# Optimization experiments

Hardware: AMD Instinct MI355X
Metric: run time of the kernel (lower is better)

## Reference

```python
import jax, jax.numpy as jnp
import numpy as np

B, S, H, SSZ, IN = 1024, 100, 128, 100, 2


def _gru(x, h, Wih, Whh, bih, bhh):
    # PyTorch GRU cell: gates ordered (reset, update, new)
    gx = x @ Wih.T + bih
    gh = h @ Whh.T + bhh
    xr, xz, xn = jnp.split(gx, 3, axis=-1)
    hr, hz, hn = jnp.split(gh, 3, axis=-1)
    r = jax.nn.sigmoid(xr + hr)
    z = jax.nn.sigmoid(xz + hz)
    n = jnp.tanh(xn + r * hn)
    return (1.0 - z) * n + z * h


def _attn(inst_h, rnn_out, W, v):
    # inst_h: [B,S,H], rnn_out: [B,H] -> softmax attention weights [B,S]
    h = jnp.concatenate([inst_h, jnp.broadcast_to(rnn_out[:, None, :], inst_h.shape)], axis=-1)
    s = jax.nn.relu(jnp.einsum('bsk,kh->bsh', h, W)) @ v
    return jax.nn.softmax(s, axis=1)


def setup_inputs() -> dict:
    key = jax.random.key(0)
    k = jax.random.split(key, 32)
    p = lambda i, shape, sc=0.05: sc * jax.random.normal(k[i], shape, jnp.float32)
    instance = jax.random.uniform(k[0], (B, S, IN), jnp.float32)
    # solutions must be per-row permutations of node indices
    solution_1 = jnp.argsort(jax.random.uniform(k[1], (B, S)), axis=1).astype(jnp.int32)
    solution_2 = jnp.argsort(jax.random.uniform(k[2], (B, S)), axis=1).astype(jnp.int32)
    eps = jax.random.normal(k[3], (B, SSZ), jnp.float32)
    return dict(
        instance=instance, solution_1=solution_1, solution_2=solution_2, eps=eps,
        emb_i_W=p(4, (H, IN)), emb_i_b=jnp.zeros(H, jnp.float32),
        emb_r_W=p(5, (H, IN)), emb_r_b=jnp.zeros(H, jnp.float32),
        attn_W=p(6, (2 * H, H)), attn_v=p(7, (H,)),
        gru_Wih=p(8, (3 * H, H)), gru_Whh=p(9, (3 * H, H)),
        gru_bih=jnp.zeros(3 * H, jnp.float32), gru_bhh=jnp.zeros(3 * H, jnp.float32),
        grud_Wih=p(10, (3 * H, 2 * H)), grud_Whh=p(11, (3 * H, H)),
        grud_bih=jnp.zeros(3 * H, jnp.float32), grud_bhh=jnp.zeros(3 * H, jnp.float32),
        enc_fc1_W=p(12, (SSZ, H)), enc_fc1_b=jnp.zeros(SSZ, jnp.float32),
        enc_fc2_W=p(13, (SSZ, H)), enc_fc2_b=jnp.zeros(SSZ, jnp.float32),
        ptr_W=p(14, (2 * H, H)), ptr_v=p(15, (H,)),
        pfc1_W=p(16, (2 * H, 2 * H + SSZ)), pfc1_b=jnp.zeros(2 * H, jnp.float32),
        pfc2_W=p(17, (H, 2 * H)), pfc2_b=jnp.zeros(H, jnp.float32),
    )


def reference(instance, solution_1, solution_2, eps,
              emb_i_W, emb_i_b, emb_r_W, emb_r_b, attn_W, attn_v,
              gru_Wih, gru_Whh, gru_bih, gru_bhh,
              grud_Wih, grud_Whh, grud_bih, grud_bhh,
              enc_fc1_W, enc_fc1_b, enc_fc2_W, enc_fc2_b,
              ptr_W, ptr_v, pfc1_W, pfc1_b, pfc2_W, pfc2_b):
    b_idx = jnp.arange(B)
    inst_h = instance @ emb_i_W.T + emb_i_b  # [B,S,H]
    emb_r = lambda x: x @ emb_r_W.T + emb_r_b
    take = lambda ptr: instance[b_idx, ptr]  # gather node coords [B,IN]

    # ---------------- Encoder ----------------
    def enc_step(carry, ptr):
        h1, h2, ref_h = carry
        h1 = _gru(ref_h, h1, gru_Wih, gru_Whh, gru_bih, gru_bhh)
        a = _attn(inst_h, h1, attn_W, attn_v)
        context = jnp.einsum('bs,bsh->bh', a, inst_h)
        ref_h = emb_r(take(ptr))
        rnn_in = jnp.concatenate([ref_h, context], axis=-1)  # [B,2H]
        h2 = _gru(rnn_in, h2, grud_Wih, grud_Whh, grud_bih, grud_bhh)
        return (h1, h2, ref_h), None

    z0 = jnp.zeros((B, H), instance.dtype)
    ref_h0 = emb_r(take(solution_1[:, 0]))
    (_, h2, _), _ = jax.lax.scan(enc_step, (z0, z0, ref_h0), solution_1[:, 1:].T)
    mu = h2 @ enc_fc1_W.T + enc_fc1_b
    log_var = h2 @ enc_fc2_W.T + enc_fc2_b
    Z = mu + eps * jnp.exp(0.5 * log_var)

    # ---------------- Decoder (teacher forcing) ----------------
    mask0 = jnp.ones((B, S), instance.dtype).at[b_idx, solution_2[:, 0]].set(0.0)

    def dec_step(carry, ptr):
        h1, ref_in, mask = carry
        ref_h = emb_r(ref_in)
        h1 = _gru(ref_h, h1, gru_Wih, gru_Whh, gru_bih, gru_bhh)
        a = _attn(inst_h, h1, attn_W, attn_v)
        context = jnp.einsum('bs,bsh->bh', a, inst_h)
        fc_in = jnp.concatenate([context, Z, ref_h], axis=-1)  # [B, 2H+SSZ]
        fc_out = (fc_in @ pfc1_W.T + pfc1_b) @ pfc2_W.T + pfc2_b  # no activation, as in torch
        hcat = jnp.concatenate([inst_h, jnp.broadcast_to(fc_out[:, None, :], inst_h.shape)], axis=-1)
        logits = jnp.tanh(jnp.einsum('bsk,kh->bsh', hcat, ptr_W)) @ ptr_v  # [B,S]
        probs = jax.nn.softmax(logits + jnp.log(mask), axis=1)
        logp = jnp.log(probs[b_idx, ptr])
        pred = jnp.argmax(probs, axis=1)
        mask = mask.at[b_idx, ptr].set(0.0)  # tsp.update_mask: mark chosen node visited
        return (h1, take(ptr), mask), (pred, logp)

    init = (z0, take(solution_2[:, 0]), mask0)
    _, (preds, logps) = jax.lax.scan(dec_step, init, solution_2[:, 1:].T)
    tour_idx = jnp.concatenate([solution_2[:, :1], preds.T.astype(solution_2.dtype)], axis=1)
    tour_logp = logps.T  # [B, S-1]
    return (mu, log_var, Z, tour_idx, tour_logp)
```

## Files before the change

### kernel.cpp

```cpp
#include <hip/hip_runtime.h>
#include <math.h>

static constexpr int NB  = 1024;
static constexpr int NS  = 100;
static constexpr int NH  = 128;
static constexpr int GPB = 2;
static constexpr int NTHR = 256;
static constexpr int NBLK = NB / GPB;

static constexpr int OUT_MU = 0;
static constexpr int OUT_LV = NB * NS;
static constexpr int OUT_Z  = 2 * NB * NS;
static constexpr int OUT_TI = 3 * NB * NS;
static constexpr int OUT_LP = 4 * NB * NS;

#define NEGF (-3.4e38f)

template<int C4>
__device__ __forceinline__ void dot2x3f(const float* __restrict__ wr0,
        const float* __restrict__ wr1, const float* __restrict__ wr2,
        const float* __restrict__ x0, const float* __restrict__ x1,
        float& r00, float& r01, float& r10, float& r11, float& r20, float& r21)
{
    const float4* W0 = reinterpret_cast<const float4*>(wr0);
    const float4* W1 = reinterpret_cast<const float4*>(wr1);
    const float4* W2 = reinterpret_cast<const float4*>(wr2);
    const float4* X0 = reinterpret_cast<const float4*>(x0);
    const float4* X1 = reinterpret_cast<const float4*>(x1);
    float a00 = 0.f, a01 = 0.f, a10 = 0.f, a11 = 0.f, a20 = 0.f, a21 = 0.f;
    #pragma unroll 8
    for (int c = 0; c < C4; ++c) {
        float4 u0 = W0[c], u1 = W1[c], u2 = W2[c];
        float4 v0 = X0[c], v1 = X1[c];
        a00 = fmaf(u0.x, v0.x, a00); a00 = fmaf(u0.y, v0.y, a00); a00 = fmaf(u0.z, v0.z, a00); a00 = fmaf(u0.w, v0.w, a00);
        a01 = fmaf(u0.x, v1.x, a01); a01 = fmaf(u0.y, v1.y, a01); a01 = fmaf(u0.z, v1.z, a01); a01 = fmaf(u0.w, v1.w, a01);
        a10 = fmaf(u1.x, v0.x, a10); a10 = fmaf(u1.y, v0.y, a10); a10 = fmaf(u1.z, v0.z, a10); a10 = fmaf(u1.w, v0.w, a10);
        a11 = fmaf(u1.x, v1.x, a11); a11 = fmaf(u1.y, v1.y, a11); a11 = fmaf(u1.z, v1.z, a11); a11 = fmaf(u1.w, v1.w, a11);
        a20 = fmaf(u2.x, v0.x, a20); a20 = fmaf(u2.y, v0.y, a20); a20 = fmaf(u2.z, v0.z, a20); a20 = fmaf(u2.w, v0.w, a20);
        a21 = fmaf(u2.x, v1.x, a21); a21 = fmaf(u2.y, v1.y, a21); a21 = fmaf(u2.z, v1.z, a21); a21 = fmaf(u2.w, v1.w, a21);
    }
    r00 = a00; r01 = a01; r10 = a10; r11 = a11; r20 = a20; r21 = a21;
}

template<int C4>
__device__ __forceinline__ void dot2f(const float* __restrict__ w,
        const float* __restrict__ x0, const float* __restrict__ x1, float& r0, float& r1)
{
    const float4* W = reinterpret_cast<const float4*>(w);
    const float4* X0 = reinterpret_cast<const float4*>(x0);
    const float4* X1 = reinterpret_cast<const float4*>(x1);
    float a0 = 0.f, a1 = 0.f;
    #pragma unroll 8
    for (int c = 0; c < C4; ++c) {
        float4 u = W[c];
        float4 v0 = X0[c], v1 = X1[c];
        a0 = fmaf(u.x, v0.x, a0); a0 = fmaf(u.y, v0.y, a0); a0 = fmaf(u.z, v0.z, a0); a0 = fmaf(u.w, v0.w, a0);
        a1 = fmaf(u.x, v1.x, a1); a1 = fmaf(u.y, v1.y, a1); a1 = fmaf(u.z, v1.z, a1); a1 = fmaf(u.w, v1.w, a1);
    }
    r0 = a0; r1 = a1;
}

template<int C4>
__device__ __forceinline__ void dot1f(const float* __restrict__ w,
        const float* __restrict__ x0, float& r0)
{
    const float4* W = reinterpret_cast<const float4*>(w);
    const float4* X0 = reinterpret_cast<const float4*>(x0);
    float a0 = 0.f;
    #pragma unroll 8
    for (int c = 0; c < C4; ++c) {
        float4 u = W[c];
        float4 v0 = X0[c];
        a0 = fmaf(u.x, v0.x, a0); a0 = fmaf(u.y, v0.y, a0); a0 = fmaf(u.z, v0.z, a0); a0 = fmaf(u.w, v0.w, a0);
    }
    r0 = a0;
}

template<int C4>
__device__ __forceinline__ double dotwd(const float* __restrict__ w, const float* __restrict__ x)
{
    const float4* W = reinterpret_cast<const float4*>(w);
    double a = 0.0;
    #pragma unroll 8
    for (int c = 0; c < C4; ++c) {
        float4 u = W[c];
        const float* p = x + 4 * c;
        a = fma((double)u.x, (double)p[0], a);
        a = fma((double)u.y, (double)p[1], a);
        a = fma((double)u.z, (double)p[2], a);
        a = fma((double)u.w, (double)p[3], a);
    }
    return a;
}

__device__ __forceinline__ void gruc(const float* __restrict__ bih, const float* __restrict__ bhh,
        const float* __restrict__ pa, const float* __restrict__ pb, float* __restrict__ h, int j)
{
    double r = 1.0 / (1.0 + exp(-(((double)pa[j]        + (double)bih[j])        + ((double)pb[j]        + (double)bhh[j]))));
    double z = 1.0 / (1.0 + exp(-(((double)pa[NH + j]   + (double)bih[NH + j])   + ((double)pb[NH + j]   + (double)bhh[NH + j]))));
    double n = tanh(((double)pa[2*NH + j] + (double)bih[2*NH + j]) + r * ((double)pb[2*NH + j] + (double)bhh[2*NH + j]));
    h[j] = (float)((1.0 - z) * n + z * (double)h[j]);
}

__global__ __launch_bounds__(NTHR) void vae_v14(
    const float* __restrict__ instance, const int* __restrict__ sol1,
    const int* __restrict__ sol2, const float* __restrict__ eps,
    const float* __restrict__ emb_i_W, const float* __restrict__ emb_i_b,
    const float* __restrict__ emb_r_W, const float* __restrict__ emb_r_b,
    const float* __restrict__ attn_W, const float* __restrict__ attn_v,
    const float* __restrict__ gru_Wih, const float* __restrict__ gru_Whh,
    const float* __restrict__ gru_bih, const float* __restrict__ gru_bhh,
    const float* __restrict__ grud_Wih, const float* __restrict__ grud_Whh,
    const float* __restrict__ grud_bih, const float* __restrict__ grud_bhh,
    const float* __restrict__ efc1_W, const float* __restrict__ efc1_b,
    const float* __restrict__ efc2_W, const float* __restrict__ efc2_b,
    const float* __restrict__ ptr_W, const float* __restrict__ ptr_v,
    const float* __restrict__ pfc1_W, const float* __restrict__ pfc1_b,
    const float* __restrict__ pfc2_W, const float* __restrict__ pfc2_b,
    float* __restrict__ out)
{
    __shared__ float  s_x[GPB][360];
    __shared__ float  s_h1[GPB][NH], s_h2[GPB][NH], s_fco[GPB][NH];
    __shared__ float  s_fch[GPB][256];
    __shared__ float  s_pa[GPB][3 * NH], s_pb[GPB][3 * NH];
    __shared__ double s_qh[GPB][NH];
    __shared__ double s_qpA[GPB][NH], s_qpB[GPB][NH];
    __shared__ double2 dAa[NH], dAp[NH];
    __shared__ double dAba[NH], dAbp[NH];
    __shared__ float  s_lg[GPB][NS], s_a[GPB][NS];
    __shared__ float  s_c0[GPB][NS], s_c1[GPB][NS], s_msk[GPB][NS];
    __shared__ float  t_wi0[NH], t_wi1[NH], t_bi[NH];
    __shared__ float  t_wr0[NH], t_wr1[NH], t_br[NH];
    __shared__ float  t_va[NH], t_vp[NH];
    __shared__ float  t_gbih[3*NH], t_gbhh[3*NH], t_dbih[3*NH], t_dbhh[3*NH];
    __shared__ float  t_p1b[256], t_p2b[NH];
    __shared__ int    s_sol1[GPB][NS], s_sol2[GPB][NS];
    __shared__ float  s_red[GPB][2];
    __shared__ double s_redd[GPB][2];
    __shared__ int    s_ri[GPB][2];
    __shared__ float  s_rc0[GPB], s_rc1[GPB];

    const int tid = threadIdx.x;
    const int bbase = blockIdx.x * GPB;
    const int j = tid & (NH - 1);
    const int half = tid >> 7;
    const int g = half;
    const int lane = tid & 63;
    const int wid = (tid >> 6) & 1;

    if (tid < NH) {
        t_wi0[tid] = emb_i_W[2*tid]; t_wi1[tid] = emb_i_W[2*tid+1]; t_bi[tid] = emb_i_b[tid];
        t_wr0[tid] = emb_r_W[2*tid]; t_wr1[tid] = emb_r_W[2*tid+1]; t_br[tid] = emb_r_b[tid];
        t_va[tid] = attn_v[tid]; t_vp[tid] = ptr_v[tid];
        t_p2b[tid] = pfc2_b[tid];
    }
    t_p1b[tid] = pfc1_b[tid];
    for (int i = tid; i < 3 * NH; i += NTHR) {
        t_gbih[i] = gru_bih[i]; t_gbhh[i] = gru_bhh[i];
        t_dbih[i] = grud_bih[i]; t_dbhh[i] = grud_bhh[i];
    }
    for (int i = tid; i < GPB * NS; i += NTHR) {
        int gg = i / NS, s = i - gg * NS;
        s_c0[gg][s] = instance[(size_t)((bbase + gg) * NS + s) * 2 + 0];
        s_c1[gg][s] = instance[(size_t)((bbase + gg) * NS + s) * 2 + 1];
        s_sol1[gg][s] = sol1[(bbase + gg) * NS + s];
        s_sol2[gg][s] = sol2[(bbase + gg) * NS + s];
    }
    s_h1[g][j] = 0.f;
    s_h2[g][j] = 0.f;
    __syncthreads();
    {
        const float* Wm = (half == 0) ? attn_W : ptr_W;
        double a0 = 0.0, a1 = 0.0, ab = 0.0;
        for (int k = 0; k < NH; ++k) {
            double wv = (double)Wm[(size_t)k * NH + j];
            a0 = fma((double)t_wi0[k], wv, a0);
            a1 = fma((double)t_wi1[k], wv, a1);
            ab = fma((double)t_bi[k],  wv, ab);
        }
        if (half == 0) { dAa[j].x = a0; dAa[j].y = a1; dAba[j] = ab; }
        else           { dAp[j].x = a0; dAp[j].y = a1; dAbp[j] = ab; }
    }
    {
        int sp = s_sol1[g][0];
        s_x[g][j] = fmaf(s_c0[g][sp], t_wr0[j], fmaf(s_c1[g][sp], t_wr1[j], t_br[j]));
    }
    __syncthreads();

    for (int t = 1; t < NS; ++t) {
        if (half == 0) {
            float a00,a01,a10,a11,a20,a21;
            dot2x3f<32>(gru_Wih + (size_t)j * NH, gru_Wih + (size_t)(NH + j) * NH,
                        gru_Wih + (size_t)(2*NH + j) * NH, s_x[0], s_x[1],
                        a00,a01,a10,a11,a20,a21);
            s_pa[0][j] = a00;        s_pa[1][j] = a01;
            s_pa[0][NH + j] = a10;   s_pa[1][NH + j] = a11;
            s_pa[0][2*NH + j] = a20; s_pa[1][2*NH + j] = a21;
        } else {
            float a00,a01,a10,a11,a20,a21;
            dot2x3f<32>(gru_Whh + (size_t)j * NH, gru_Whh + (size_t)(NH + j) * NH,
                        gru_Whh + (size_t)(2*NH + j) * NH, s_h1[0], s_h1[1],
                        a00,a01,a10,a11,a20,a21);
            s_pb[0][j] = a00;        s_pb[1][j] = a01;
            s_pb[0][NH + j] = a10;   s_pb[1][NH + j] = a11;
            s_pb[0][2*NH + j] = a20; s_pb[1][2*NH + j] = a21;
        }
        __syncthreads();
        gruc(t_gbih, t_gbhh, s_pa[g], s_pb[g], s_h1[g], j);
        __syncthreads();
        {
            const float* col = attn_W + (size_t)NH * NH + j;
            const int k0 = half * 64;
            double a00=0.0,a01=0.0,a02=0.0,a03=0.0;
            double a10=0.0,a11=0.0,a12=0.0,a13=0.0;
            #pragma unroll 8
            for (int k = 0; k < 64; k += 4) {
                float w0 = col[(size_t)(k0+k+0) * NH];
                float w1 = col[(size_t)(k0+k+1) * NH];
                float w2 = col[(size_t)(k0+k+2) * NH];
                float w3 = col[(size_t)(k0+k+3) * NH];
                float4 h0 = *reinterpret_cast<const float4*>(&s_h1[0][k0+k]);
                float4 h1v = *reinterpret_cast<const float4*>(&s_h1[1][k0+k]);
                a00 = fma((double)w0, (double)h0.x, a00);
                a01 = fma((double)w1, (double)h0.y, a01);
                a02 = fma((double)w2, (double)h0.z, a02);
                a03 = fma((double)w3, (double)h0.w, a03);
                a10 = fma((double)w0, (double)h1v.x, a10);
                a11 = fma((double)w1, (double)h1v.y, a11);
                a12 = fma((double)w2, (double)h1v.z, a12);
                a13 = fma((double)w3, (double)h1v.w, a13);
            }
            if (half == 0) { s_qpA[0][j] = (a00+a01)+(a02+a03); s_qpA[1][j] = (a10+a11)+(a12+a13); }
            else           { s_qpB[0][j] = (a00+a01)+(a02+a03); s_qpB[1][j] = (a10+a11)+(a12+a13); }
        }
        __syncthreads();
        s_qh[g][j] = dAba[j] + (s_qpA[g][j] + s_qpB[g][j]);
        __syncthreads();
        if (j < NS) {
            double c00 = (double)s_c0[g][j], c10 = (double)s_c1[g][j];
            double acc0 = 0.0, acc1 = 0.0, acc2 = 0.0, acc3 = 0.0;
            #pragma unroll 4
            for (int h = 0; h < NH; h += 4) {
                double2 A0 = dAa[h+0], A1 = dAa[h+1], A2 = dAa[h+2], A3 = dAa[h+3];
                double p0 = fma(c00, A0.x, fma(c10, A0.y, s_qh[g][h+0]));
                double p1 = fma(c00, A1.x, fma(c10, A1.y, s_qh[g][h+1]));
                double p2 = fma(c00, A2.x, fma(c10, A2.y, s_qh[g][h+2]));
                double p3 = fma(c00, A3.x, fma(c10, A3.y, s_qh[g][h+3]));
                acc0 = fma(fmax(p0, 0.0), (double)t_va[h+0], acc0);
                acc1 = fma(fmax(p1, 0.0), (double)t_va[h+1], acc1);
                acc2 = fma(fmax(p2, 0.0), (double)t_va[h+2], acc2);
                acc3 = fma(fmax(p3, 0.0), (double)t_va[h+3], acc3);
            }
            s_lg[g][j] = (float)(((acc0 + acc1) + (acc2 + acc3)));
        }
        __syncthreads();
        {
            float a = s_lg[g][lane];
            float b = (lane + 64 < NS) ? s_lg[g][lane + 64] : NEGF;
            float m = fmaxf(a, b);
            m = fmaxf(m, __shfl_xor(m, 32)); m = fmaxf(m, __shfl_xor(m, 16));
            m = fmaxf(m, __shfl_xor(m, 8));  m = fmaxf(m, __shfl_xor(m, 4));
            m = fmaxf(m, __shfl_xor(m, 2));  m = fmaxf(m, __shfl_xor(m, 1));
            float fv = 0.f;
            if (j < NS) { fv = (float)exp((double)s_lg[g][j] - (double)m); s_a[g][j] = fv; }
            double ps = (double)fv;
            ps += __shfl_xor(ps, 32); ps += __shfl_xor(ps, 16);
            ps += __shfl_xor(ps, 8);  ps += __shfl_xor(ps, 4);
            ps += __shfl_xor(ps, 2);  ps += __shfl_xor(ps, 1);
            if (lane == 0) s_redd[g][wid] = ps;
        }
        __syncthreads();
        if (j < NS) {
            double se = s_redd[g][0] + s_redd[g][1];
            s_a[g][j] = (float)((double)s_a[g][j] / se);
        }
        __syncthreads();
        {
            float w0 = t_wi0[j], w1 = t_wi1[j], bb = t_bi[j];
            double a0 = 0.0, a1 = 0.0, a2 = 0.0, a3 = 0.0;
            #pragma unroll 5
            for (int s = 0; s < NS; s += 4) {
                float ih0 = fmaf(s_c0[g][s+0], w0, fmaf(s_c1[g][s+0], w1, bb));
                float ih1 = fmaf(s_c0[g][s+1], w0, fmaf(s_c1[g][s+1], w1, bb));
                float ih2 = fmaf(s_c0[g][s+2], w0, fmaf(s_c1[g][s+2], w1, bb));
                float ih3 = fmaf(s_c0[g][s+3], w0, fmaf(s_c1[g][s+3], w1, bb));
                a0 += (double)s_a[g][s+0] * (double)ih0;
                a1 += (double)s_a[g][s+1] * (double)ih1;
                a2 += (double)s_a[g][s+2] * (double)ih2;
                a3 += (double)s_a[g][s+3] * (double)ih3;
            }
            s_x[g][NH + j] = (float)(((a0 + a1) + (a2 + a3)));
            int sp = s_sol1[g][t];
            s_x[g][j] = fmaf(s_c0[g][sp], t_wr0[j], fmaf(s_c1[g][sp], t_wr1[j], t_br[j]));
        }
        __syncthreads();
        if (half == 0) {
            float a00,a01,a10,a11,a20,a21;
            dot2x3f<64>(grud_Wih + (size_t)j * 256, grud_Wih + (size_t)(NH + j) * 256,
                        grud_Wih + (size_t)(2*NH + j) * 256, s_x[0], s_x[1],
                        a00,a01,a10,a11,a20,a21);
            s_pa[0][j] = a00;        s_pa[1][j] = a01;
            s_pa[0][NH + j] = a10;   s_pa[1][NH + j] = a11;
            s_pa[0][2*NH + j] = a20; s_pa[1][2*NH + j] = a21;
        } else {
            float a00,a01,a10,a11,a20,a21;
            dot2x3f<32>(grud_Whh + (size_t)j * NH, grud_Whh + (size_t)(NH + j) * NH,
                        grud_Whh + (size_t)(2*NH + j) * NH, s_h2[0], s_h2[1],
                        a00,a01,a10,a11,a20,a21);
            s_pb[0][j] = a00;        s_pb[1][j] = a01;
            s_pb[0][NH + j] = a10;   s_pb[1][NH + j] = a11;
            s_pb[0][2*NH + j] = a20; s_pb[1][2*NH + j] = a21;
        }
        __syncthreads();
        gruc(t_dbih, t_dbhh, s_pa[g], s_pb[g], s_h2[g], j);
        __syncthreads();
    }

    for (int idx = tid; idx < GPB * NS; idx += NTHR) {
        int gg = idx / NS, s = idx - gg * NS, b = bbase + gg;
        double mu = dotwd<32>(efc1_W + (size_t)s * NH, s_h2[gg]) + (double)efc1_b[s];
        double lv = dotwd<32>(efc2_W + (size_t)s * NH, s_h2[gg]) + (double)efc2_b[s];
        double z  = mu + (double)eps[(size_t)b * NS + s] * exp(0.5 * lv);
        out[OUT_MU + b * NS + s] = (float)mu;
        out[OUT_LV + b * NS + s] = (float)lv;
        out[OUT_Z  + b * NS + s] = (float)z;
        s_x[gg][NH + s] = (float)z;
    }
    for (int i = tid; i < GPB * NS; i += NTHR) {
        int gg = i / NS, s = i - gg * NS;
        s_msk[gg][s] = 1.f;
    }
    s_h1[g][j] = 0.f;
    __syncthreads();
    if (tid < GPB) {
        int b = bbase + tid;
        int s0 = s_sol2[tid][0];
        s_msk[tid][s0] = 0.f;
        s_rc0[tid] = s_c0[tid][s0];
        s_rc1[tid] = s_c1[tid][s0];
        out[OUT_TI + b * NS + 0] = (float)s0;
    }
    __syncthreads();

    for (int t = 1; t < NS; ++t) {
        s_x[g][228 + j] = fmaf(s_rc0[g], t_wr0[j], fmaf(s_rc1[g], t_wr1[j], t_br[j]));
        __syncthreads();
        if (half == 0) {
            float a00,a01,a10,a11,a20,a21;
            dot2x3f<32>(gru_Wih + (size_t)j * NH, gru_Wih + (size_t)(NH + j) * NH,
                        gru_Wih + (size_t)(2*NH + j) * NH, s_x[0]+228, s_x[1]+228,
                        a00,a01,a10,a11,a20,a21);
            s_pa[0][j] = a00;        s_pa[1][j] = a01;
            s_pa[0][NH + j] = a10;   s_pa[1][NH + j] = a11;
            s_pa[0][2*NH + j] = a20; s_pa[1][2*NH + j] = a21;
        } else {
            float a00,a01,a10,a11,a20,a21;
            dot2x3f<32>(gru_Whh + (size_t)j * NH, gru_Whh + (size_t)(NH + j) * NH,
                        gru_Whh + (size_t)(2*NH + j) * NH, s_h1[0], s_h1[1],
                        a00,a01,a10,a11,a20,a21);
            s_pb[0][j] = a00;        s_pb[1][j] = a01;
            s_pb[0][NH + j] = a10;   s_pb[1][NH + j] = a11;
            s_pb[0][2*NH + j] = a20; s_pb[1][2*NH + j] = a21;
        }
        __syncthreads();
        gruc(t_gbih, t_gbhh, s_pa[g], s_pb[g], s_h1[g], j);
        __syncthreads();
        {
            const float* col = attn_W + (size_t)NH * NH + j;
            const int k0 = half * 64;
            double a00=0.0,a01=0.0,a02=0.0,a03=0.0;
            double a10=0.0,a11=0.0,a12=0.0,a13=0.0;
            #pragma unroll 8
            for (int k = 0; k < 64; k += 4) {
                float w0 = col[(size_t)(k0+k+0) * NH];
                float w1 = col[(size_t)(k0+k+1) * NH];
                float w2 = col[(size_t)(k0+k+2) * NH];
                float w3 = col[(size_t)(k0+k+3) * NH];
                float4 h0 = *reinterpret_cast<const float4*>(&s_h1[0][k0+k]);
                float4 h1v = *reinterpret_cast<const float4*>(&s_h1[1][k0+k]);
                a00 = fma((double)w0, (double)h0.x, a00);
                a01 = fma((double)w1, (double)h0.y, a01);
                a02 = fma((double)w2, (double)h0.z, a02);
                a03 = fma((double)w3, (double)h0.w, a03);
                a10 = fma((double)w0, (double)h1v.x, a10);
                a11 = fma((double)w1, (double)h1v.y, a11);
                a12 = fma((double)w2, (double)h1v.z, a12);
                a13 = fma((double)w3, (double)h1v.w, a13);
            }
            if (half == 0) { s_qpA[0][j] = (a00+a01)+(a02+a03); s_qpA[1][j] = (a10+a11)+(a12+a13); }
            else           { s_qpB[0][j] = (a00+a01)+(a02+a03); s_qpB[1][j] = (a10+a11)+(a12+a13); }
        }
        __syncthreads();
        s_qh[g][j] = dAba[j] + (s_qpA[g][j] + s_qpB[g][j]);
        __syncthreads();
        if (j < NS) {
            double c00 = (double)s_c0[g][j], c10 = (double)s_c1[g][j];
            double acc0 = 0.0, acc1 = 0.0, acc2 = 0.0, acc3 = 0.0;
            #pragma unroll 4
            for (int h = 0; h < NH; h += 4) {
                double2 A0 = dAa[h+0], A1 = dAa[h+1], A2 = dAa[h+2], A3 = dAa[h+3];
                double p0 = fma(c00, A0.x, fma(c10, A0.y, s_qh[g][h+0]));
                double p1 = fma(c00, A1.x, fma(c10, A1.y, s_qh[g][h+1]));
                double p2 = fma(c00, A2.x, fma(c10, A2.y, s_qh[g][h+2]));
                double p3 = fma(c00, A3.x, fma(c10, A3.y, s_qh[g][h+3]));
                acc0 = fma(fmax(p0, 0.0), (double)t_va[h+0], acc0);
                acc1 = fma(fmax(p1, 0.0), (double)t_va[h+1], acc1);
                acc2 = fma(fmax(p2, 0.0), (double)t_va[h+2], acc2);
                acc3 = fma(fmax(p3, 0.0), (double)t_va[h+3], acc3);
            }
            s_lg[g][j] = (float)(((acc0 + acc1) + (acc2 + acc3)));
        }
        __syncthreads();
        {
            float a = s_lg[g][lane];
            float b = (lane + 64 < NS) ? s_lg[g][lane + 64] : NEGF;
            float m = fmaxf(a, b);
            m = fmaxf(m, __shfl_xor(m, 32)); m = fmaxf(m, __shfl_xor(m, 16));
            m = fmaxf(m, __shfl_xor(m, 8));  m = fmaxf(m, __shfl_xor(m, 4));
            m = fmaxf(m, __shfl_xor(m, 2));  m = fmaxf(m, __shfl_xor(m, 1));
            float fv = 0.f;
            if (j < NS) { fv = (float)exp((double)s_lg[g][j] - (double)m); s_a[g][j] = fv; }
            double ps = (double)fv;
            ps += __shfl_xor(ps, 32); ps += __shfl_xor(ps, 16);
            ps += __shfl_xor(ps, 8);  ps += __shfl_xor(ps, 4);
            ps += __shfl_xor(ps, 2);  ps += __shfl_xor(ps, 1);
            if (lane == 0) s_redd[g][wid] = ps;
        }
        __syncthreads();
        if (j < NS) {
            double se = s_redd[g][0] + s_redd[g][1];
            s_a[g][j] = (float)((double)s_a[g][j] / se);
        }
        __syncthreads();
        {
            float w0 = t_wi0[j], w1 = t_wi1[j], bb = t_bi[j];
            double a0 = 0.0, a1 = 0.0, a2 = 0.0, a3 = 0.0;
            #pragma unroll 5
            for (int s = 0; s < NS; s += 4) {
                float ih0 = fmaf(s_c0[g][s+0], w0, fmaf(s_c1[g][s+0], w1, bb));
                float ih1 = fmaf(s_c0[g][s+1], w0, fmaf(s_c1[g][s+1], w1, bb));
                float ih2 = fmaf(s_c0[g][s+2], w0, fmaf(s_c1[g][s+2], w1, bb));
                float ih3 = fmaf(s_c0[g][s+3], w0, fmaf(s_c1[g][s+3], w1, bb));
                a0 += (double)s_a[g][s+0] * (double)ih0;
                a1 += (double)s_a[g][s+1] * (double)ih1;
                a2 += (double)s_a[g][s+2] * (double)ih2;
                a3 += (double)s_a[g][s+3] * (double)ih3;
            }
            s_x[g][j] = (float)(((a0 + a1) + (a2 + a3)));
        }
        __syncthreads();
        {
            float r0, r1;
            dot2f<89>(pfc1_W + (size_t)tid * 356, s_x[0], s_x[1], r0, r1);
            float bb = t_p1b[tid];
            s_fch[0][tid] = r0 + bb; s_fch[1][tid] = r1 + bb;
        }
        __syncthreads();
        {
            float r0;
            dot1f<64>(pfc2_W + (size_t)j * 256, s_fch[g], r0);
            s_fco[g][j] = r0 + t_p2b[j];
        }
        __syncthreads();
        {
            const float* col = ptr_W + (size_t)NH * NH + j;
            const int k0 = half * 64;
            double a00=0.0,a01=0.0,a02=0.0,a03=0.0;
            double a10=0.0,a11=0.0,a12=0.0,a13=0.0;
            #pragma unroll 8
            for (int k = 0; k < 64; k += 4) {
                float w0 = col[(size_t)(k0+k+0) * NH];
                float w1 = col[(size_t)(k0+k+1) * NH];
                float w2 = col[(size_t)(k0+k+2) * NH];
                float w3 = col[(size_t)(k0+k+3) * NH];
                float4 f0 = *reinterpret_cast<const float4*>(&s_fco[0][k0+k]);
                float4 f1 = *reinterpret_cast<const float4*>(&s_fco[1][k0+k]);
                a00 = fma((double)w0, (double)f0.x, a00);
                a01 = fma((double)w1, (double)f0.y, a01);
                a02 = fma((double)w2, (double)f0.z, a02);
                a03 = fma((double)w3, (double)f0.w, a03);
                a10 = fma((double)w0, (double)f1.x, a10);
                a11 = fma((double)w1, (double)f1.y, a11);
                a12 = fma((double)w2, (double)f1.z, a12);
                a13 = fma((double)w3, (double)f1.w, a13);
            }
            if (half == 0) { s_qpA[0][j] = (a00+a01)+(a02+a03); s_qpA[1][j] = (a10+a11)+(a12+a13); }
            else           { s_qpB[0][j] = (a00+a01)+(a02+a03); s_qpB[1][j] = (a10+a11)+(a12+a13); }
        }
        __syncthreads();
        s_qh[g][j] = dAbp[j] + (s_qpA[g][j] + s_qpB[g][j]);
        __syncthreads();
        if (j < NS) {
            double c00 = (double)s_c0[g][j], c10 = (double)s_c1[g][j];
            double acc0 = 0.0, acc1 = 0.0, acc2 = 0.0, acc3 = 0.0;
            #pragma unroll 4
            for (int h = 0; h < NH; h += 4) {
                double2 A0 = dAp[h+0], A1 = dAp[h+1], A2 = dAp[h+2], A3 = dAp[h+3];
                double p0 = fma(c00, A0.x, fma(c10, A0.y, s_qh[g][h+0]));
                double p1 = fma(c00, A1.x, fma(c10, A1.y, s_qh[g][h+1]));
                double p2 = fma(c00, A2.x, fma(c10, A2.y, s_qh[g][h+2]));
                double p3 = fma(c00, A3.x, fma(c10, A3.y, s_qh[g][h+3]));
                acc0 = fma((double)tanhf((float)p0), (double)t_vp[h+0], acc0);
                acc1 = fma((double)tanhf((float)p1), (double)t_vp[h+1], acc1);
                acc2 = fma((double)tanhf((float)p2), (double)t_vp[h+2], acc2);
                acc3 = fma((double)tanhf((float)p3), (double)t_vp[h+3], acc3);
            }
            s_lg[g][j] = (float)(((acc0 + acc1) + (acc2 + acc3)));
        }
        __syncthreads();
        {
            float la = s_lg[g][lane];
            float ma = (s_msk[g][lane] > 0.f) ? la : NEGF;
            float lb = NEGF;
            if (lane + 64 < NS) lb = (s_msk[g][lane + 64] > 0.f) ? s_lg[g][lane + 64] : NEGF;
            float m = fmaxf(ma, lb);
            m = fmaxf(m, __shfl_xor(m, 32)); m = fmaxf(m, __shfl_xor(m, 16));
            m = fmaxf(m, __shfl_xor(m, 8));  m = fmaxf(m, __shfl_xor(m, 4));
            m = fmaxf(m, __shfl_xor(m, 2));  m = fmaxf(m, __shfl_xor(m, 1));
            float fv = 0.f;
            if (j < NS) {
                fv = (s_msk[g][j] > 0.f) ? (float)exp((double)s_lg[g][j] - (double)m) : 0.f;
                s_a[g][j] = fv;
            }
            float  bv = (j < NS) ? fv : -1.f;
            int    bi = (j < NS) ? j  : NS;
            double ps = (j < NS) ? (double)fv : 0.0;
            #pragma unroll
            for (int o = 32; o >= 1; o >>= 1) {
                float  ov = __shfl_xor(bv, o);
                int    oi = __shfl_xor(bi, o);
                double op = __shfl_xor(ps, o);
                ps += op;
                if (ov > bv || (ov == bv && oi < bi)) { bv = ov; bi = oi; }
            }
            if (lane == 0) { s_red[g][wid] = bv; s_ri[g][wid] = bi; s_redd[g][wid] = ps; }
        }
        __syncthreads();
        if (tid < GPB) {
            int gg = tid, b = bbase + gg;
            float m = -1.f; int mi = NS; double se = 0.0;
            for (int i = 0; i < 2; ++i) {
                se += s_redd[gg][i];
                float v = s_red[gg][i]; int vi = s_ri[gg][i];
                if (v > m || (v == m && vi < mi)) { m = v; mi = vi; }
            }
            int pt = s_sol2[gg][t];
            double logp = log((double)s_a[gg][pt] / se);
            out[OUT_TI + b * NS + t]             = (float)mi;
            out[OUT_LP + b * (NS - 1) + (t - 1)] = (float)logp;
            s_msk[gg][pt] = 0.f;
            s_rc0[gg] = s_c0[gg][pt];
            s_rc1[gg] = s_c1[gg][pt];
        }
        __syncthreads();
    }
}

extern "C" void kernel_launch(void* const* d_in, const int* in_sizes, int n_in,
                              void* d_out, int out_size, void* d_ws, size_t ws_size,
                              hipStream_t stream)
{
    (void)in_sizes; (void)n_in; (void)out_size; (void)d_ws; (void)ws_size;
    vae_v14<<<NBLK, NTHR, 0, stream>>>(
        (const float*)d_in[0], (const int*)d_in[1], (const int*)d_in[2], (const float*)d_in[3],
        (const float*)d_in[4], (const float*)d_in[5], (const float*)d_in[6], (const float*)d_in[7],
        (const float*)d_in[8], (const float*)d_in[9], (const float*)d_in[10], (const float*)d_in[11],
        (const float*)d_in[12], (const float*)d_in[13], (const float*)d_in[14], (const float*)d_in[15],
        (const float*)d_in[16], (const float*)d_in[17], (const float*)d_in[18], (const float*)d_in[19],
        (const float*)d_in[20], (const float*)d_in[21], (const float*)d_in[22], (const float*)d_in[23],
        (const float*)d_in[24], (const float*)d_in[25], (const float*)d_in[26], (const float*)d_in[27],
        (float*)d_out);
}
```

Baseline: 12.26 ms.

## Process one batch element per block and split per-step work across both thread halves

The kernel now handles one batch row per 256-thread block instead of two, launching twice as many blocks. With the second row gone, the two thread halves split the remaining work: the decoder GRU hidden matvec overlaps with the encoder GRU cell update, and the attention and pointer score loops are divided over the hidden dimension, with partial sums combined in shared memory. This is meant to raise parallelism per step and remove serial phases, but it gives up reuse of each weight load across two rows, so global and L2 weight traffic per batch element roughly doubles.

```diff
diff --git a/kernel.cpp b/kernel.cpp
--- a/kernel.cpp
+++ b/kernel.cpp
@@ -4,9 +4,8 @@
 static constexpr int NB  = 1024;
 static constexpr int NS  = 100;
 static constexpr int NH  = 128;
-static constexpr int GPB = 2;
 static constexpr int NTHR = 256;
-static constexpr int NBLK = NB / GPB;
+static constexpr int NBLK = NB;
 
 static constexpr int OUT_MU = 0;
 static constexpr int OUT_LV = NB * NS;
@@ -17,47 +16,24 @@
 #define NEGF (-3.4e38f)
 
 template<int C4>
-__device__ __forceinline__ void dot2x3f(const float* __restrict__ wr0,
+__device__ __forceinline__ void dot1x3f(const float* __restrict__ wr0,
         const float* __restrict__ wr1, const float* __restrict__ wr2,
-        const float* __restrict__ x0, const float* __restrict__ x1,
-        float& r00, float& r01, float& r10, float& r11, float& r20, float& r21)
+        const float* __restrict__ x, float& r0, float& r1, float& r2)
 {
     const float4* W0 = reinterpret_cast<const float4*>(wr0);
     const float4* W1 = reinterpret_cast<const float4*>(wr1);
     const float4* W2 = reinterpret_cast<const float4*>(wr2);
-    const float4* X0 = reinterpret_cast<const float4*>(x0);
-    const float4* X1 = reinterpret_cast<const float4*>(x1);
-    float a00 = 0.f, a01 = 0.f, a10 = 0.f, a11 = 0.f, a20 = 0.f, a21 = 0.f;
+    const float4* X  = reinterpret_cast<const float4*>(x);
+    float a0 = 0.f, a1 = 0.f, a2 = 0.f;
     #pragma unroll 8
     for (int c = 0; c < C4; ++c) {
         float4 u0 = W0[c], u1 = W1[c], u2 = W2[c];
-        float4 v0 = X0[c], v1 = X1[c];
-        a00 = fmaf(u0.x, v0.x, a00); a00 = fmaf(u0.y, v0.y, a00); a00 = fmaf(u0.z, v0.z, a00); a00 = fmaf(u0.w, v0.w, a00);
-        a01 = fmaf(u0.x, v1.x, a01); a01 = fmaf(u0.y, v1.y, a01); a01 = fmaf(u0.z, v1.z, a01); a01 = fmaf(u0.w, v1.w, a01);
-        a10 = fmaf(u1.x, v0.x, a10); a10 = fmaf(u1.y, v0.y, a10); a10 = fmaf(u1.z, v0.z, a10); a10 = fmaf(u1.w, v0.w, a10);
-        a11 = fmaf(u1.x, v1.x, a11); a11 = fmaf(u1.y, v1.y, a11); a11 = fmaf(u1.z, v1.z, a11); a11 = fmaf(u1.w, v1.w, a11);
-        a20 = fmaf(u2.x, v0.x, a20); a20 = fmaf(u2.y, v0.y, a20); a20 = fmaf(u2.z, v0.z, a20); a20 = fmaf(u2.w, v0.w, a20);
-        a21 = fmaf(u2.x, v1.x, a21); a21 = fmaf(u2.y, v1.y, a21); a21 = fmaf(u2.z, v1.z, a21); a21 = fmaf(u2.w, v1.w, a21);
-    }
-    r00 = a00; r01 = a01; r10 = a10; r11 = a11; r20 = a20; r21 = a21;
-}
-
-template<int C4>
-__device__ __forceinline__ void dot2f(const float* __restrict__ w,
-        const float* __restrict__ x0, const float* __restrict__ x1, float& r0, float& r1)
-{
-    const float4* W = reinterpret_cast<const float4*>(w);
-    const float4* X0 = reinterpret_cast<const float4*>(x0);
-    const float4* X1 = reinterpret_cast<const float4*>(x1);
-    float a0 = 0.f, a1 = 0.f;
-    #pragma unroll 8
-    for (int c = 0; c < C4; ++c) {
-        float4 u = W[c];
-        float4 v0 = X0[c], v1 = X1[c];
-        a0 = fmaf(u.x, v0.x, a0); a0 = fmaf(u.y, v0.y, a0); a0 = fmaf(u.z, v0.z, a0); a0 = fmaf(u.w, v0.w, a0);
-        a1 = fmaf(u.x, v1.x, a1); a1 = fmaf(u.y, v1.y, a1); a1 = fmaf(u.z, v1.z, a1); a1 = fmaf(u.w, v1.w, a1);
-    }
-    r0 = a0; r1 = a1;
+        float4 v = X[c];
+        a0 = fmaf(u0.x, v.x, a0); a0 = fmaf(u0.y, v.y, a0); a0 = fmaf(u0.z, v.z, a0); a0 = fmaf(u0.w, v.w, a0);
+        a1 = fmaf(u1.x, v.x, a1); a1 = fmaf(u1.y, v.y, a1); a1 = fmaf(u1.z, v.z, a1); a1 = fmaf(u1.w, v.w, a1);
+        a2 = fmaf(u2.x, v.x, a2); a2 = fmaf(u2.y, v.y, a2); a2 = fmaf(u2.z, v.z, a2); a2 = fmaf(u2.w, v.w, a2);
+    }
+    r0 = a0; r1 = a1; r2 = a2;
 }
 
 template<int C4>
@@ -102,7 +78,7 @@
     h[j] = (float)((1.0 - z) * n + z * (double)h[j]);
 }
 
-__global__ __launch_bounds__(NTHR) void vae_v14(
+__global__ __launch_bounds__(NTHR) void vae_v16(
     const float* __restrict__ instance, const int* __restrict__ sol1,
     const int* __restrict__ sol2, const float* __restrict__ eps,
     const float* __restrict__ emb_i_W, const float* __restrict__ emb_i_b,
@@ -119,34 +95,34 @@
     const float* __restrict__ pfc2_W, const float* __restrict__ pfc2_b,
     float* __restrict__ out)
 {
-    __shared__ float  s_x[GPB][360];
-    __shared__ float  s_h1[GPB][NH], s_h2[GPB][NH], s_fco[GPB][NH];
-    __shared__ float  s_fch[GPB][256];
-    __shared__ float  s_pa[GPB][3 * NH], s_pb[GPB][3 * NH];
-    __shared__ double s_qh[GPB][NH];
-    __shared__ double s_qpA[GPB][NH], s_qpB[GPB][NH];
+    __shared__ __align__(16) float s_x[360];
+    __shared__ __align__(16) float s_h1[NH], s_h2[NH], s_fco[NH];
+    __shared__ __align__(16) float s_fch[256];
+    __shared__ float  s_pa1[3*NH], s_pb1[3*NH];
+    __shared__ float  s_pa2[3*NH], s_pb2[3*NH];
+    __shared__ double s_qpA[NH], s_qpB[NH];
+    __shared__ double s_hpA[NH], s_hpB[NH];
     __shared__ double2 dAa[NH], dAp[NH];
     __shared__ double dAba[NH], dAbp[NH];
-    __shared__ float  s_lg[GPB][NS], s_a[GPB][NS];
-    __shared__ float  s_c0[GPB][NS], s_c1[GPB][NS], s_msk[GPB][NS];
+    __shared__ float  s_a[NS], s_msk[NS];
+    __shared__ float  s_c0[NS], s_c1[NS];
     __shared__ float  t_wi0[NH], t_wi1[NH], t_bi[NH];
     __shared__ float  t_wr0[NH], t_wr1[NH], t_br[NH];
     __shared__ float  t_va[NH], t_vp[NH];
     __shared__ float  t_gbih[3*NH], t_gbhh[3*NH], t_dbih[3*NH], t_dbhh[3*NH];
     __shared__ float  t_p1b[256], t_p2b[NH];
-    __shared__ int    s_sol1[GPB][NS], s_sol2[GPB][NS];
-    __shared__ float  s_red[GPB][2];
-    __shared__ double s_redd[GPB][2];
-    __shared__ int    s_ri[GPB][2];
-    __shared__ float  s_rc0[GPB], s_rc1[GPB];
-
-    const int tid = threadIdx.x;
-    const int bbase = blockIdx.x * GPB;
-    const int j = tid & (NH - 1);
+    __shared__ int    s_sol1[NS], s_sol2[NS];
+    __shared__ double s_redd[2];
+    __shared__ float  s_red[2];
+    __shared__ int    s_ri[2];
+    __shared__ float  s_rc0, s_rc1;
+
+    const int tid  = threadIdx.x;
+    const int b    = blockIdx.x;
+    const int j2   = tid & (NH - 1);
     const int half = tid >> 7;
-    const int g = half;
     const int lane = tid & 63;
-    const int wid = (tid >> 6) & 1;
+    const int wid  = (tid >> 6) & 1;
 
     if (tid < NH) {
         t_wi0[tid] = emb_i_W[2*tid]; t_wi1[tid] = emb_i_W[2*tid+1]; t_bi[tid] = emb_i_b[tid];
@@ -159,372 +135,359 @@
         t_gbih[i] = gru_bih[i]; t_gbhh[i] = gru_bhh[i];
         t_dbih[i] = grud_bih[i]; t_dbhh[i] = grud_bhh[i];
     }
-    for (int i = tid; i < GPB * NS; i += NTHR) {
-        int gg = i / NS, s = i - gg * NS;
-        s_c0[gg][s] = instance[(size_t)((bbase + gg) * NS + s) * 2 + 0];
-        s_c1[gg][s] = instance[(size_t)((bbase + gg) * NS + s) * 2 + 1];
-        s_sol1[gg][s] = sol1[(bbase + gg) * NS + s];
-        s_sol2[gg][s] = sol2[(bbase + gg) * NS + s];
-    }
-    s_h1[g][j] = 0.f;
-    s_h2[g][j] = 0.f;
+    if (tid < NS) {
+        s_c0[tid] = instance[(size_t)(b * NS + tid) * 2 + 0];
+        s_c1[tid] = instance[(size_t)(b * NS + tid) * 2 + 1];
+        s_sol1[tid] = sol1[b * NS + tid];
+        s_sol2[tid] = sol2[b * NS + tid];
+    }
+    if (tid < NH) { s_h1[tid] = 0.f; s_h2[tid] = 0.f; }
     __syncthreads();
     {
         const float* Wm = (half == 0) ? attn_W : ptr_W;
         double a0 = 0.0, a1 = 0.0, ab = 0.0;
         for (int k = 0; k < NH; ++k) {
-            double wv = (double)Wm[(size_t)k * NH + j];
+            double wv = (double)Wm[(size_t)k * NH + j2];
             a0 = fma((double)t_wi0[k], wv, a0);
             a1 = fma((double)t_wi1[k], wv, a1);
             ab = fma((double)t_bi[k],  wv, ab);
         }
-        if (half == 0) { dAa[j].x = a0; dAa[j].y = a1; dAba[j] = ab; }
-        else           { dAp[j].x = a0; dAp[j].y = a1; dAbp[j] = ab; }
-    }
-    {
-        int sp = s_sol1[g][0];
-        s_x[g][j] = fmaf(s_c0[g][sp], t_wr0[j], fmaf(s_c1[g][sp], t_wr1[j], t_br[j]));
+        if (half == 0) { dAa[j2].x = a0; dAa[j2].y = a1; dAba[j2] = ab; }
+        else           { dAp[j2].x = a0; dAp[j2].y = a1; dAbp[j2] = ab; }
+    }
+    if (tid < NH) {
+        int sp = s_sol1[0];
+        s_x[tid] = fmaf(s_c0[sp], t_wr0[tid], fmaf(s_c1[sp], t_wr1[tid], t_br[tid]));
     }
     __syncthreads();
 
     for (int t = 1; t < NS; ++t) {
         if (half == 0) {
-            float a00,a01,a10,a11,a20,a21;
-            dot2x3f<32>(gru_Wih + (size_t)j * NH, gru_Wih + (size_t)(NH + j) * NH,
-                        gru_Wih + (size_t)(2*NH + j) * NH, s_x[0], s_x[1],
-                        a00,a01,a10,a11,a20,a21);
-            s_pa[0][j] = a00;        s_pa[1][j] = a01;
-            s_pa[0][NH + j] = a10;   s_pa[1][NH + j] = a11;
-            s_pa[0][2*NH + j] = a20; s_pa[1][2*NH + j] = a21;
+            float r0, r1, r2;
+            dot1x3f<32>(gru_Wih + (size_t)j2 * NH, gru_Wih + (size_t)(NH + j2) * NH,
+                        gru_Wih + (size_t)(2*NH + j2) * NH, s_x, r0, r1, r2);
+            s_pa1[j2] = r0; s_pa1[NH + j2] = r1; s_pa1[2*NH + j2] = r2;
         } else {
-            float a00,a01,a10,a11,a20,a21;
-            dot2x3f<32>(gru_Whh + (size_t)j * NH, gru_Whh + (size_t)(NH + j) * NH,
-                        gru_Whh + (size_t)(2*NH + j) * NH, s_h1[0], s_h1[1],
-                        a00,a01,a10,a11,a20,a21);
-            s_pb[0][j] = a00;        s_pb[1][j] = a01;
-            s_pb[0][NH + j] = a10;   s_pb[1][NH + j] = a11;
-            s_pb[0][2*NH + j] = a20; s_pb[1][2*NH + j] = a21;
-        }
-        __syncthreads();
-        gruc(t_gbih, t_gbhh, s_pa[g], s_pb[g], s_h1[g], j);
+            float r0, r1, r2;
+            dot1x3f<32>(gru_Whh + (size_t)j2 * NH, gru_Whh + (size_t)(NH + j2) * NH,
+                        gru_Whh + (size_t)(2*NH + j2) * NH, s_h1, r0, r1, r2);
+            s_pb1[j2] = r0; s_pb1[NH + j2] = r1; s_pb1[2*NH + j2] = r2;
+        }
+        __syncthreads();
+        if (half == 0) {
+            gruc(t_gbih, t_gbhh, s_pa1, s_pb1, s_h1, j2);
+        } else {
+            float r0, r1, r2;
+            dot1x3f<32>(grud_Whh + (size_t)j2 * NH, grud_Whh + (size_t)(NH + j2) * NH,
+                        grud_Whh + (size_t)(2*NH + j2) * NH, s_h2, r0, r1, r2);
+            s_pb2[j2] = r0; s_pb2[NH + j2] = r1; s_pb2[2*NH + j2] = r2;
+        }
         __syncthreads();
         {
-            const float* col = attn_W + (size_t)NH * NH + j;
+            const float* col = attn_W + (size_t)NH * NH + j2;
             const int k0 = half * 64;
-            double a00=0.0,a01=0.0,a02=0.0,a03=0.0;
-            double a10=0.0,a11=0.0,a12=0.0,a13=0.0;
+            double a0=0.0,a1=0.0,a2=0.0,a3=0.0;
             #pragma unroll 8
             for (int k = 0; k < 64; k += 4) {
                 float w0 = col[(size_t)(k0+k+0) * NH];
                 float w1 = col[(size_t)(k0+k+1) * NH];
                 float w2 = col[(size_t)(k0+k+2) * NH];
                 float w3 = col[(size_t)(k0+k+3) * NH];
-                float4 h0 = *reinterpret_cast<const float4*>(&s_h1[0][k0+k]);
-                float4 h1v = *reinterpret_cast<const float4*>(&s_h1[1][k0+k]);
-                a00 = fma((double)w0, (double)h0.x, a00);
-                a01 = fma((double)w1, (double)h0.y, a01);
-                a02 = fma((double)w2, (double)h0.z, a02);
-                a03 = fma((double)w3, (double)h0.w, a03);
-                a10 = fma((double)w0, (double)h1v.x, a10);
-                a11 = fma((double)w1, (double)h1v.y, a11);
-                a12 = fma((double)w2, (double)h1v.z, a12);
-                a13 = fma((double)w3, (double)h1v.w, a13);
-            }
-            if (half == 0) { s_qpA[0][j] = (a00+a01)+(a02+a03); s_qpA[1][j] = (a10+a11)+(a12+a13); }
-            else           { s_qpB[0][j] = (a00+a01)+(a02+a03); s_qpB[1][j] = (a10+a11)+(a12+a13); }
-        }
-        __syncthreads();
-        s_qh[g][j] = dAba[j] + (s_qpA[g][j] + s_qpB[g][j]);
-        __syncthreads();
-        if (j < NS) {
-            double c00 = (double)s_c0[g][j], c10 = (double)s_c1[g][j];
-            double acc0 = 0.0, acc1 = 0.0, acc2 = 0.0, acc3 = 0.0;
+                float4 h0 = *reinterpret_cast<const float4*>(&s_h1[k0+k]);
+                a0 = fma((double)w0, (double)h0.x, a0);
+                a1 = fma((double)w1, (double)h0.y, a1);
+                a2 = fma((double)w2, (double)h0.z, a2);
+                a3 = fma((double)w3, (double)h0.w, a3);
+            }
+            if (half == 0) s_qpA[j2] = (a0+a1)+(a2+a3);
+            else           s_qpB[j2] = (a0+a1)+(a2+a3);
+        }
+        __syncthreads();
+        if (j2 < NS) {
+            double c00 = (double)s_c0[j2], c10 = (double)s_c1[j2];
+            const int h0 = half * 64;
+            double acc0=0.0,acc1=0.0,acc2=0.0,acc3=0.0;
             #pragma unroll 4
-            for (int h = 0; h < NH; h += 4) {
-                double2 A0 = dAa[h+0], A1 = dAa[h+1], A2 = dAa[h+2], A3 = dAa[h+3];
-                double p0 = fma(c00, A0.x, fma(c10, A0.y, s_qh[g][h+0]));
-                double p1 = fma(c00, A1.x, fma(c10, A1.y, s_qh[g][h+1]));
-                double p2 = fma(c00, A2.x, fma(c10, A2.y, s_qh[g][h+2]));
-                double p3 = fma(c00, A3.x, fma(c10, A3.y, s_qh[g][h+3]));
-                acc0 = fma(fmax(p0, 0.0), (double)t_va[h+0], acc0);
-                acc1 = fma(fmax(p1, 0.0), (double)t_va[h+1], acc1);
-                acc2 = fma(fmax(p2, 0.0), (double)t_va[h+2], acc2);
-                acc3 = fma(fmax(p3, 0.0), (double)t_va[h+3], acc3);
-            }
-            s_lg[g][j] = (float)(((acc0 + acc1) + (acc2 + acc3)));
-        }
-        __syncthreads();
-        {
-            float a = s_lg[g][lane];
-            float b = (lane + 64 < NS) ? s_lg[g][lane + 64] : NEGF;
-            float m = fmaxf(a, b);
+            for (int hh = 0; hh < 64; hh += 4) {
+                const int h = h0 + hh;
+                double2 A0=dAa[h+0],A1=dAa[h+1],A2=dAa[h+2],A3=dAa[h+3];
+                double q0 = dAba[h+0] + (s_qpA[h+0]+s_qpB[h+0]);
+                double q1 = dAba[h+1] + (s_qpA[h+1]+s_qpB[h+1]);
+                double q2v= dAba[h+2] + (s_qpA[h+2]+s_qpB[h+2]);
+                double q3 = dAba[h+3] + (s_qpA[h+3]+s_qpB[h+3]);
+                double p0 = fma(c00,A0.x,fma(c10,A0.y,q0));
+                double p1 = fma(c00,A1.x,fma(c10,A1.y,q1));
+                double p2 = fma(c00,A2.x,fma(c10,A2.y,q2v));
+                double p3 = fma(c00,A3.x,fma(c10,A3.y,q3));
+                acc0 = fma(fmax(p0,0.0),(double)t_va[h+0],acc0);
+                acc1 = fma(fmax(p1,0.0),(double)t_va[h+1],acc1);
+                acc2 = fma(fmax(p2,0.0),(double)t_va[h+2],acc2);
+                acc3 = fma(fmax(p3,0.0),(double)t_va[h+3],acc3);
+            }
+            double pr = (acc0+acc1)+(acc2+acc3);
+            if (half == 0) s_hpA[j2] = pr; else s_hpB[j2] = pr;
+        }
+        __syncthreads();
+        if (tid < 128) {
+            float a = (float)(s_hpA[lane] + s_hpB[lane]);
+            float bb = (lane + 64 < NS) ? (float)(s_hpA[lane+64] + s_hpB[lane+64]) : NEGF;
+            float m = fmaxf(a, bb);
             m = fmaxf(m, __shfl_xor(m, 32)); m = fmaxf(m, __shfl_xor(m, 16));
             m = fmaxf(m, __shfl_xor(m, 8));  m = fmaxf(m, __shfl_xor(m, 4));
             m = fmaxf(m, __shfl_xor(m, 2));  m = fmaxf(m, __shfl_xor(m, 1));
+            float lgj = wid ? bb : a;
             float fv = 0.f;
-            if (j < NS) { fv = (float)exp((double)s_lg[g][j] - (double)m); s_a[g][j] = fv; }
+            if (j2 < NS) { fv = (float)exp((double)lgj - (double)m); s_a[j2] = fv; }
             double ps = (double)fv;
             ps += __shfl_xor(ps, 32); ps += __shfl_xor(ps, 16);
             ps += __shfl_xor(ps, 8);  ps += __shfl_xor(ps, 4);
             ps += __shfl_xor(ps, 2);  ps += __shfl_xor(ps, 1);
-            if (lane == 0) s_redd[g][wid] = ps;
-        }
-        __syncthreads();
-        if (j < NS) {
-            double se = s_redd[g][0] + s_redd[g][1];
-            s_a[g][j] = (float)((double)s_a[g][j] / se);
-        }
-        __syncthreads();
-        {
-            float w0 = t_wi0[j], w1 = t_wi1[j], bb = t_bi[j];
+            if (lane == 0) s_redd[wid] = ps;
+        }
+        __syncthreads();
+        if (tid < NS) {
+            double se = s_redd[0] + s_redd[1];
+            s_a[tid] = (float)((double)s_a[tid] / se);
+        }
+        __syncthreads();
+        if (half == 0) {
+            float w0 = t_wi0[j2], w1 = t_wi1[j2], bbv = t_bi[j2];
             double a0 = 0.0, a1 = 0.0, a2 = 0.0, a3 = 0.0;
             #pragma unroll 5
             for (int s = 0; s < NS; s += 4) {
-                float ih0 = fmaf(s_c0[g][s+0], w0, fmaf(s_c1[g][s+0], w1, bb));
-                float ih1 = fmaf(s_c0[g][s+1], w0, fmaf(s_c1[g][s+1], w1, bb));
-                float ih2 = fmaf(s_c0[g][s+2], w0, fmaf(s_c1[g][s+2], w1, bb));
-                float ih3 = fmaf(s_c0[g][s+3], w0, fmaf(s_c1[g][s+3], w1, bb));
-                a0 += (double)s_a[g][s+0] * (double)ih0;
-                a1 += (double)s_a[g][s+1] * (double)ih1;
-                a2 += (double)s_a[g][s+2] * (double)ih2;
-                a3 += (double)s_a[g][s+3] * (double)ih3;
-            }
-            s_x[g][NH + j] = (float)(((a0 + a1) + (a2 + a3)));
-            int sp = s_sol1[g][t];
-            s_x[g][j] = fmaf(s_c0[g][sp], t_wr0[j], fmaf(s_c1[g][sp], t_wr1[j], t_br[j]));
-        }
-        __syncthreads();
-        if (half == 0) {
-            float a00,a01,a10,a11,a20,a21;
-            dot2x3f<64>(grud_Wih + (size_t)j * 256, grud_Wih + (size_t)(NH + j) * 256,
-                        grud_Wih + (size_t)(2*NH + j) * 256, s_x[0], s_x[1],
-                        a00,a01,a10,a11,a20,a21);
-            s_pa[0][j] = a00;        s_pa[1][j] = a01;
-            s_pa[0][NH + j] = a10;   s_pa[1][NH + j] = a11;
-            s_pa[0][2*NH + j] = a20; s_pa[1][2*NH + j] = a21;
-        } else {
-            float a00,a01,a10,a11,a20,a21;
-            dot2x3f<32>(grud_Whh + (size_t)j * NH, grud_Whh + (size_t)(NH + j) * NH,
-                        grud_Whh + (size_t)(2*NH + j) * NH, s_h2[0], s_h2[1],
-                        a00,a01,a10,a11,a20,a21);
-            s_pb[0][j] = a00;        s_pb[1][j] = a01;
-            s_pb[0][NH + j] = a10;   s_pb[1][NH + j] = a11;
-            s_pb[0][2*NH + j] = a20; s_pb[1][2*NH + j] = a21;
-        }
-        __syncthreads();
-        gruc(t_dbih, t_dbhh, s_pa[g], s_pb[g], s_h2[g], j);
-        __syncthreads();
-    }
-
-    for (int idx = tid; idx < GPB * NS; idx += NTHR) {
-        int gg = idx / NS, s = idx - gg * NS, b = bbase + gg;
-        double mu = dotwd<32>(efc1_W + (size_t)s * NH, s_h2[gg]) + (double)efc1_b[s];
-        double lv = dotwd<32>(efc2_W + (size_t)s * NH, s_h2[gg]) + (double)efc2_b[s];
+                float ih0 = fmaf(s_c0[s+0], w0, fmaf(s_c1[s+0], w1, bbv));
+                float ih1 = fmaf(s_c0[s+1], w0, fmaf(s_c1[s+1], w1, bbv));
+                float ih2 = fmaf(s_c0[s+2], w0, fmaf(s_c1[s+2], w1, bbv));
+                float ih3 = fmaf(s_c0[s+3], w0, fmaf(s_c1[s+3], w1, bbv));
+                a0 += (double)s_a[s+0] * (double)ih0;
+                a1 += (double)s_a[s+1] * (double)ih1;
+                a2 += (double)s_a[s+2] * (double)ih2;
+                a3 += (double)s_a[s+3] * (double)ih3;
+            }
+            s_x[NH + j2] = (float)(((a0 + a1) + (a2 + a3)));
+            int sp = s_sol1[t];
+            s_x[j2] = fmaf(s_c0[sp], t_wr0[j2], fmaf(s_c1[sp], t_wr1[j2], t_br[j2]));
+        }
+        __syncthreads();
+        {
+            float r;
+            dot1f<64>(grud_Wih + (size_t)tid * 256, s_x, r);
+            s_pa2[tid] = r;
+            if (tid >= 128) {
+                float r2;
+                dot1f<64>(grud_Wih + (size_t)(256 + (tid - 128)) * 256, s_x, r2);
+                s_pa2[256 + (tid - 128)] = r2;
+            }
+        }
+        __syncthreads();
+        if (tid < 128) gruc(t_dbih, t_dbhh, s_pa2, s_pb2, s_h2, j2);
+        __syncthreads();
+    }
+
+    if (tid < NS) {
+        int s = tid;
+        double mu = dotwd<32>(efc1_W + (size_t)s * NH, s_h2) + (double)efc1_b[s];
+        double lv = dotwd<32>(efc2_W + (size_t)s * NH, s_h2) + (double)efc2_b[s];
         double z  = mu + (double)eps[(size_t)b * NS + s] * exp(0.5 * lv);
         out[OUT_MU + b * NS + s] = (float)mu;
         out[OUT_LV + b * NS + s] = (float)lv;
         out[OUT_Z  + b * NS + s] = (float)z;
-        s_x[gg][NH + s] = (float)z;
-    }
-    for (int i = tid; i < GPB * NS; i += NTHR) {
-        int gg = i / NS, s = i - gg * NS;
-        s_msk[gg][s] = 1.f;
-    }
-    s_h1[g][j] = 0.f;
+        s_x[NH + s] = (float)z;
+        s_msk[s] = 1.f;
+    }
+    if (tid < NH) s_h1[tid] = 0.f;
     __syncthreads();
-    if (tid < GPB) {
-        int b = bbase + tid;
-        int s0 = s_sol2[tid][0];
-        s_msk[tid][s0] = 0.f;
-        s_rc0[tid] = s_c0[tid][s0];
-        s_rc1[tid] = s_c1[tid][s0];
+    if (tid == 0) {
+        int s0 = s_sol2[0];
+        s_msk[s0] = 0.f;
+        s_rc0 = s_c0[s0];
+        s_rc1 = s_c1[s0];
         out[OUT_TI + b * NS + 0] = (float)s0;
     }
     __syncthreads();
 
     for (int t = 1; t < NS; ++t) {
-        s_x[g][228 + j] = fmaf(s_rc0[g], t_wr0[j], fmaf(s_rc1[g], t_wr1[j], t_br[j]));
+        if (tid < 128) s_x[228 + tid] = fmaf(s_rc0, t_wr0[tid], fmaf(s_rc1, t_wr1[tid], t_br[tid]));
         __syncthreads();
         if (half == 0) {
-            float a00,a01,a10,a11,a20,a21;
-            dot2x3f<32>(gru_Wih + (size_t)j * NH, gru_Wih + (size_t)(NH + j) * NH,
-                        gru_Wih + (size_t)(2*NH + j) * NH, s_x[0]+228, s_x[1]+228,
-                        a00,a01,a10,a11,a20,a21);
-            s_pa[0][j] = a00;        s_pa[1][j] = a01;
-            s_pa[0][NH + j] = a10;   s_pa[1][NH + j] = a11;
-            s_pa[0][2*NH + j] = a20; s_pa[1][2*NH + j] = a21;
+            float r0, r1, r2;
+            dot1x3f<32>(gru_Wih + (size_t)j2 * NH, gru_Wih + (size_t)(NH + j2) * NH,
+                        gru_Wih + (size_t)(2*NH + j2) * NH, s_x + 228, r0, r1, r2);
+            s_pa1[j2] = r0; s_pa1[NH + j2] = r1; s_pa1[2*NH + j2] = r2;
         } else {
-            float a00,a01,a10,a11,a20,a21;
-            dot2x3f<32>(gru_Whh + (size_t)j * NH, gru_Whh + (size_t)(NH + j) * NH,
-                        gru_Whh + (size_t)(2*NH + j) * NH, s_h1[0], s_h1[1],
-                        a00,a01,a10,a11,a20,a21);
-            s_pb[0][j] = a00;        s_pb[1][j] = a01;
-            s_pb[0][NH + j] = a10;   s_pb[1][NH + j] = a11;
-            s_pb[0][2*NH + j] = a20; s_pb[1][2*NH + j] = a21;
-        }
-        __syncthreads();
-        gruc(t_gbih, t_gbhh, s_pa[g], s_pb[g], s_h1[g], j);
+            float r0, r1, r2;
+            dot1x3f<32>(gru_Whh + (size_t)j2 * NH, gru_Whh + (size_t)(NH + j2) * NH,
+                        gru_Whh + (size_t)(2*NH + j2) * NH, s_h1, r0, r1, r2);
+            s_pb1[j2] = r0; s_pb1[NH + j2] = r1; s_pb1[2*NH + j2] = r2;
+        }
+        __syncthreads();
+        if (tid < 128) gruc(t_gbih, t_gbhh, s_pa1, s_pb1, s_h1, j2);
         __syncthreads();
         {
-            const float* col = attn_W + (size_t)NH * NH + j;
+            const float* col = attn_W + (size_t)NH * NH + j2;
             const int k0 = half * 64;
-            double a00=0.0,a01=0.0,a02=0.0,a03=0.0;
-            double a10=0.0,a11=0.0,a12=0.0,a13=0.0;
+            double a0=0.0,a1=0.0,a2=0.0,a3=0.0;
             #pragma unroll 8
             for (int k = 0; k < 64; k += 4) {
                 float w0 = col[(size_t)(k0+k+0) * NH];
                 float w1 = col[(size_t)(k0+k+1) * NH];
                 float w2 = col[(size_t)(k0+k+2) * NH];
                 float w3 = col[(size_t)(k0+k+3) * NH];
-                float4 h0 = *reinterpret_cast<const float4*>(&s_h1[0][k0+k]);
-                float4 h1v = *reinterpret_cast<const float4*>(&s_h1[1][k0+k]);
-                a00 = fma((double)w0, (double)h0.x, a00);
-                a01 = fma((double)w1, (double)h0.y, a01);
-                a02 = fma((double)w2, (double)h0.z, a02);
-                a03 = fma((double)w3, (double)h0.w, a03);
-                a10 = fma((double)w0, (double)h1v.x, a10);
-                a11 = fma((double)w1, (double)h1v.y, a11);
-                a12 = fma((double)w2, (double)h1v.z, a12);
-                a13 = fma((double)w3, (double)h1v.w, a13);
-            }
-            if (half == 0) { s_qpA[0][j] = (a00+a01)+(a02+a03); s_qpA[1][j] = (a10+a11)+(a12+a13); }
-            else           { s_qpB[0][j] = (a00+a01)+(a02+a03); s_qpB[1][j] = (a10+a11)+(a12+a13); }
-        }
-        __syncthreads();
-        s_qh[g][j] = dAba[j] + (s_qpA[g][j] + s_qpB[g][j]);
-        __syncthreads();
-        if (j < NS) {
-            double c00 = (double)s_c0[g][j], c10 = (double)s_c1[g][j];
-            double acc0 = 0.0, acc1 = 0.0, acc2 = 0.0, acc3 = 0.0;
+                float4 h0 = *reinterpret_cast<const float4*>(&s_h1[k0+k]);
+                a0 = fma((double)w0, (double)h0.x, a0);
+                a1 = fma((double)w1, (double)h0.y, a1);
+                a2 = fma((double)w2, (double)h0.z, a2);
+                a3 = fma((double)w3, (double)h0.w, a3);
+            }
+            if (half == 0) s_qpA[j2] = (a0+a1)+(a2+a3);
+            else           s_qpB[j2] = (a0+a1)+(a2+a3);
+        }
+        __syncthreads();
+        if (j2 < NS) {
+            double c00 = (double)s_c0[j2], c10 = (double)s_c1[j2];
+            const int h0 = half * 64;
+            double acc0=0.0,acc1=0.0,acc2=0.0,acc3=0.0;
             #pragma unroll 4
-            for (int h = 0; h < NH; h += 4) {
-                double2 A0 = dAa[h+0], A1 = dAa[h+1], A2 = dAa[h+2], A3 = dAa[h+3];
-                double p0 = fma(c00, A0.x, fma(c10, A0.y, s_qh[g][h+0]));
-                double p1 = fma(c00, A1.x, fma(c10, A1.y, s_qh[g][h+1]));
-                double p2 = fma(c00, A2.x, fma(c10, A2.y, s_qh[g][h+2]));
-                double p3 = fma(c00, A3.x, fma(c10, A3.y, s_qh[g][h+3]));
-                acc0 = fma(fmax(p0, 0.0), (double)t_va[h+0], acc0);
-                acc1 = fma(fmax(p1, 0.0), (double)t_va[h+1], acc1);
-                acc2 = fma(fmax(p2, 0.0), (double)t_va[h+2], acc2);
-                acc3 = fma(fmax(p3, 0.0), (double)t_va[h+3], acc3);
-            }
-            s_lg[g][j] = (float)(((acc0 + acc1) + (acc2 + acc3)));
-        }
-        __syncthreads();
-        {
-            float a = s_lg[g][lane];
-            float b = (lane + 64 < NS) ? s_lg[g][lane + 64] : NEGF;
-            float m = fmaxf(a, b);
+            for (int hh = 0; hh < 64; hh += 4) {
+                const int h = h0 + hh;
+                double2 A0=dAa[h+0],A1=dAa[h+1],A2=dAa[h+2],A3=dAa[h+3];
+                double q0 = dAba[h+0] + (s_qpA[h+0]+s_qpB[h+0]);
+                double q1 = dAba[h+1] + (s_qpA[h+1]+s_qpB[h+1]);
+                double q2v= dAba[h+2] + (s_qpA[h+2]+s_qpB[h+2]);
+                double q3 = dAba[h+3] + (s_qpA[h+3]+s_qpB[h+3]);
+                double p0 = fma(c00,A0.x,fma(c10,A0.y,q0));
+                double p1 = fma(c00,A1.x,fma(c10,A1.y,q1));
+                double p2 = fma(c00,A2.x,fma(c10,A2.y,q2v));
+                double p3 = fma(c00,A3.x,fma(c10,A3.y,q3));
+                acc0 = fma(fmax(p0,0.0),(double)t_va[h+0],acc0);
+                acc1 = fma(fmax(p1,0.0),(double)t_va[h+1],acc1);
+                acc2 = fma(fmax(p2,0.0),(double)t_va[h+2],acc2);
+                acc3 = fma(fmax(p3,0.0),(double)t_va[h+3],acc3);
+            }
+            double pr = (acc0+acc1)+(acc2+acc3);
+            if (half == 0) s_hpA[j2] = pr; else s_hpB[j2] = pr;
+        }
+        __syncthreads();
+        if (tid < 128) {
+            float a = (float)(s_hpA[lane] + s_hpB[lane]);
+            float bb = (lane + 64 < NS) ? (float)(s_hpA[lane+64] + s_hpB[lane+64]) : NEGF;
+            float m = fmaxf(a, bb);
             m = fmaxf(m, __shfl_xor(m, 32)); m = fmaxf(m, __shfl_xor(m, 16));
             m = fmaxf(m, __shfl_xor(m, 8));  m = fmaxf(m, __shfl_xor(m, 4));
             m = fmaxf(m, __shfl_xor(m, 2));  m = fmaxf(m, __shfl_xor(m, 1));
+            float lgj = wid ? bb : a;
             float fv = 0.f;
-            if (j < NS) { fv = (float)exp((double)s_lg[g][j] - (double)m); s_a[g][j] = fv; }
+            if (j2 < NS) { fv = (float)exp((double)lgj - (double)m); s_a[j2] = fv; }
             double ps = (double)fv;
             ps += __shfl_xor(ps, 32); ps += __shfl_xor(ps, 16);
             ps += __shfl_xor(ps, 8);  ps += __shfl_xor(ps, 4);
             ps += __shfl_xor(ps, 2);  ps += __shfl_xor(ps, 1);
-            if (lane == 0) s_redd[g][wid] = ps;
-        }
-        __syncthreads();
-        if (j < NS) {
-            double se = s_redd[g][0] + s_redd[g][1];
-            s_a[g][j] = (float)((double)s_a[g][j] / se);
-        }
-        __syncthreads();
-        {
-            float w0 = t_wi0[j], w1 = t_wi1[j], bb = t_bi[j];
+            if (lane == 0) s_redd[wid] = ps;
+        }
+        __syncthreads();
+        if (tid < NS) {
+            double se = s_redd[0] + s_redd[1];
+            s_a[tid] = (float)((double)s_a[tid] / se);
+        }
+        __syncthreads();
+        if (half == 0) {
+            float w0 = t_wi0[j2], w1 = t_wi1[j2], bbv = t_bi[j2];
             double a0 = 0.0, a1 = 0.0, a2 = 0.0, a3 = 0.0;
             #pragma unroll 5
             for (int s = 0; s < NS; s += 4) {
-                float ih0 = fmaf(s_c0[g][s+0], w0, fmaf(s_c1[g][s+0], w1, bb));
-                float ih1 = fmaf(s_c0[g][s+1], w0, fmaf(s_c1[g][s+1], w1, bb));
-                float ih2 = fmaf(s_c0[g][s+2], w0, fmaf(s_c1[g][s+2], w1, bb));
-                float ih3 = fmaf(s_c0[g][s+3], w0, fmaf(s_c1[g][s+3], w1, bb));
-                a0 += (double)s_a[g][s+0] * (double)ih0;
-                a1 += (double)s_a[g][s+1] * (double)ih1;
-                a2 += (double)s_a[g][s+2] * (double)ih2;
-                a3 += (double)s_a[g][s+3] * (double)ih3;
-            }
-            s_x[g][j] = (float)(((a0 + a1) + (a2 + a3)));
+                float ih0 = fmaf(s_c0[s+0], w0, fmaf(s_c1[s+0], w1, bbv));
+                float ih1 = fmaf(s_c0[s+1], w0, fmaf(s_c1[s+1], w1, bbv));
+                float ih2 = fmaf(s_c0[s+2], w0, fmaf(s_c1[s+2], w1, bbv));
+                float ih3 = fmaf(s_c0[s+3], w0, fmaf(s_c1[s+3], w1, bbv));
+                a0 += (double)s_a[s+0] * (double)ih0;
+                a1 += (double)s_a[s+1] * (double)ih1;
+                a2 += (double)s_a[s+2] * (double)ih2;
+                a3 += (double)s_a[s+3] * (double)ih3;
+            }
+            s_x[j2] = (float)(((a0 + a1) + (a2 + a3)));
         }
         __syncthreads();
         {
-            float r0, r1;
-            dot2f<89>(pfc1_W + (size_t)tid * 356, s_x[0], s_x[1], r0, r1);
-            float bb = t_p1b[tid];
-            s_fch[0][tid] = r0 + bb; s_fch[1][tid] = r1 + bb;
+            float r;
+            dot1f<89>(pfc1_W + (size_t)tid * 356, s_x, r);
+            s_fch[tid] = r + t_p1b[tid];
+        }
+        __syncthreads();
+        if (tid < 128) {
+            float r;
+            dot1f<64>(pfc2_W + (size_t)j2 * 256, s_fch, r);
+            s_fco[j2] = r + t_p2b[j2];
         }
         __syncthreads();
         {
-            float r0;
-            dot1f<64>(pfc2_W + (size_t)j * 256, s_fch[g], r0);
-            s_fco[g][j] = r0 + t_p2b[j];
-        }
-        __syncthreads();
-        {
-            const float* col = ptr_W + (size_t)NH * NH + j;
+            const float* col = ptr_W + (size_t)NH * NH + j2;
             const int k0 = half * 64;
-            double a00=0.0,a01=0.0,a02=0.0,a03=0.0;
-            double a10=0.0,a11=0.0,a12=0.0,a13=0.0;
+            double a0=0.0,a1=0.0,a2=0.0,a3=0.0;
             #pragma unroll 8
             for (int k = 0; k < 64; k += 4) {
                 float w0 = col[(size_t)(k0+k+0) * NH];
                 float w1 = col[(size_t)(k0+k+1) * NH];
                 float w2 = col[(size_t)(k0+k+2) * NH];
                 float w3 = col[(size_t)(k0+k+3) * NH];
-                float4 f0 = *reinterpret_cast<const float4*>(&s_fco[0][k0+k]);
-                float4 f1 = *reinterpret_cast<const float4*>(&s_fco[1][k0+k]);
-                a00 = fma((double)w0, (double)f0.x, a00);
-                a01 = fma((double)w1, (double)f0.y, a01);
-                a02 = fma((double)w2, (double)f0.z, a02);
-                a03 = fma((double)w3, (double)f0.w, a03);
-                a10 = fma((double)w0, (double)f1.x, a10);
-                a11 = fma((double)w1, (double)f1.y, a11);
-                a12 = fma((double)w2, (double)f1.z, a12);
-                a13 = fma((double)w3, (double)f1.w, a13);
-            }
-            if (half == 0) { s_qpA[0][j] = (a00+a01)+(a02+a03); s_qpA[1][j] = (a10+a11)+(a12+a13); }
-            else           { s_qpB[0][j] = (a00+a01)+(a02+a03); s_qpB[1][j] = (a10+a11)+(a12+a13); }
-        }
-        __syncthreads();
-        s_qh[g][j] = dAbp[j] + (s_qpA[g][j] + s_qpB[g][j]);
-        __syncthreads();
-        if (j < NS) {
-            double c00 = (double)s_c0[g][j], c10 = (double)s_c1[g][j];
-            double acc0 = 0.0, acc1 = 0.0, acc2 = 0.0, acc3 = 0.0;
+                float4 f0 = *reinterpret_cast<const float4*>(&s_fco[k0+k]);
+                a0 = fma((double)w0, (double)f0.x, a0);
+                a1 = fma((double)w1, (double)f0.y, a1);
+                a2 = fma((double)w2, (double)f0.z, a2);
+                a3 = fma((double)w3, (double)f0.w, a3);
+            }
+            if (half == 0) s_qpA[j2] = (a0+a1)+(a2+a3);
+            else           s_qpB[j2] = (a0+a1)+(a2+a3);
+        }
+        __syncthreads();
+        if (j2 < NS) {
+            double c00 = (double)s_c0[j2], c10 = (double)s_c1[j2];
+            const int h0 = half * 64;
+            double acc0=0.0,acc1=0.0,acc2=0.0,acc3=0.0;
             #pragma unroll 4
-            for (int h = 0; h < NH; h += 4) {
-                double2 A0 = dAp[h+0], A1 = dAp[h+1], A2 = dAp[h+2], A3 = dAp[h+3];
-                double p0 = fma(c00, A0.x, fma(c10, A0.y, s_qh[g][h+0]));
-                double p1 = fma(c00, A1.x, fma(c10, A1.y, s_qh[g][h+1]));
-                double p2 = fma(c00, A2.x, fma(c10, A2.y, s_qh[g][h+2]));
-                double p3 = fma(c00, A3.x, fma(c10, A3.y, s_qh[g][h+3]));
-                acc0 = fma((double)tanhf((float)p0), (double)t_vp[h+0], acc0);
-                acc1 = fma((double)tanhf((float)p1), (double)t_vp[h+1], acc1);
-                acc2 = fma((double)tanhf((float)p2), (double)t_vp[h+2], acc2);
-                acc3 = fma((double)tanhf((float)p3), (double)t_vp[h+3], acc3);
-            }
-            s_lg[g][j] = (float)(((acc0 + acc1) + (acc2 + acc3)));
-        }
-        __syncthreads();
-        {
-            float la = s_lg[g][lane];
-            float ma = (s_msk[g][lane] > 0.f) ? la : NEGF;
-            float lb = NEGF;
-            if (lane + 64 < NS) lb = (s_msk[g][lane + 64] > 0.f) ? s_lg[g][lane + 64] : NEGF;
-            float m = fmaxf(ma, lb);
+            for (int hh = 0; hh < 64; hh += 4) {
+                const int h = h0 + hh;
+                double2 A0=dAp[h+0],A1=dAp[h+1],A2=dAp[h+2],A3=dAp[h+3];
+                double q0 = dAbp[h+0] + (s_qpA[h+0]+s_qpB[h+0]);
+                double q1 = dAbp[h+1] + (s_qpA[h+1]+s_qpB[h+1]);
+                double q2v= dAbp[h+2] + (s_qpA[h+2]+s_qpB[h+2]);
+                double q3 = dAbp[h+3] + (s_qpA[h+3]+s_qpB[h+3]);
+                double p0 = fma(c00,A0.x,fma(c10,A0.y,q0));
+                double p1 = fma(c00,A1.x,fma(c10,A1.y,q1));
+                double p2 = fma(c00,A2.x,fma(c10,A2.y,q2v));
+                double p3 = fma(c00,A3.x,fma(c10,A3.y,q3));
+                acc0 = fma((double)tanhf((float)p0),(double)t_vp[h+0],acc0);
+                acc1 = fma((double)tanhf((float)p1),(double)t_vp[h+1],acc1);
+                acc2 = fma((double)tanhf((float)p2),(double)t_vp[h+2],acc2);
+                acc3 = fma((double)tanhf((float)p3),(double)t_vp[h+3],acc3);
+            }
+            double pr = (acc0+acc1)+(acc2+acc3);
+            if (half == 0) s_hpA[j2] = pr; else s_hpB[j2] = pr;
+        }
+        __syncthreads();
+        if (tid < 128) {
+            float l1 = (float)(s_hpA[lane] + s_hpB[lane]);
+            bool u1 = s_msk[lane] > 0.f;
+            float c1v = u1 ? l1 : NEGF;
+            bool u2 = false; float l2 = 0.f, c2v = NEGF;
+            if (lane + 64 < NS) {
+                l2 = (float)(s_hpA[lane+64] + s_hpB[lane+64]);
+                u2 = s_msk[lane + 64] > 0.f;
+                c2v = u2 ? l2 : NEGF;
+            }
+            float m = fmaxf(c1v, c2v);
             m = fmaxf(m, __shfl_xor(m, 32)); m = fmaxf(m, __shfl_xor(m, 16));
             m = fmaxf(m, __shfl_xor(m, 8));  m = fmaxf(m, __shfl_xor(m, 4));
             m = fmaxf(m, __shfl_xor(m, 2));  m = fmaxf(m, __shfl_xor(m, 1));
-            float fv = 0.f;
-            if (j < NS) {
-                fv = (s_msk[g][j] > 0.f) ? (float)exp((double)s_lg[g][j] - (double)m) : 0.f;
-                s_a[g][j] = fv;
-            }
-            float  bv = (j < NS) ? fv : -1.f;
-            int    bi = (j < NS) ? j  : NS;
-            double ps = (j < NS) ? (double)fv : 0.0;
+            float f1 = u1 ? (float)exp((double)l1 - (double)m) : 0.f;
+            s_a[lane] = f1;
+            float f2 = 0.f;
+            if (lane + 64 < NS) {
+                f2 = u2 ? (float)exp((double)l2 - (double)m) : 0.f;
+                s_a[lane + 64] = f2;
+            }
+            float bv = f1; int bi = lane;
+            if (lane + 64 < NS && f2 > bv) { bv = f2; bi = lane + 64; }
+            double ps = (double)f1 + (double)f2;
             #pragma unroll
             for (int o = 32; o >= 1; o >>= 1) {
                 float  ov = __shfl_xor(bv, o);
@@ -533,24 +496,23 @@
                 ps += op;
                 if (ov > bv || (ov == bv && oi < bi)) { bv = ov; bi = oi; }
             }
-            if (lane == 0) { s_red[g][wid] = bv; s_ri[g][wid] = bi; s_redd[g][wid] = ps; }
-        }
-        __syncthreads();
-        if (tid < GPB) {
-            int gg = tid, b = bbase + gg;
+            if (lane == 0) { s_red[wid] = bv; s_ri[wid] = bi; s_redd[wid] = ps; }
+        }
+        __syncthreads();
+        if (tid == 0) {
             float m = -1.f; int mi = NS; double se = 0.0;
             for (int i = 0; i < 2; ++i) {
-                se += s_redd[gg][i];
-                float v = s_red[gg][i]; int vi = s_ri[gg][i];
+                se += s_redd[i];
+                float v = s_red[i]; int vi = s_ri[i];
                 if (v > m || (v == m && vi < mi)) { m = v; mi = vi; }
             }
-            int pt = s_sol2[gg][t];
-            double logp = log((double)s_a[gg][pt] / se);
-            out[OUT_TI + b * NS + t]             = (float)mi;
-            out[OUT_LP + b * (NS - 1) + (t - 1)] = (float)logp;
-            s_msk[gg][pt] = 0.f;
-            s_rc0[gg] = s_c0[gg][pt];
-            s_rc1[gg] = s_c1[gg][pt];
+            int pt = s_sol2[t];
+            double logp = log((double)s_a[pt] / se);
+            out[OUT_TI + (size_t)b * NS + t]             = (float)mi;
+            out[OUT_LP + (size_t)b * (NS - 1) + (t - 1)] = (float)logp;
+            s_msk[pt] = 0.f;
+            s_rc0 = s_c0[pt];
+            s_rc1 = s_c1[pt];
         }
         __syncthreads();
     }
@@ -561,7 +523,7 @@
                               hipStream_t stream)
 {
     (void)in_sizes; (void)n_in; (void)out_size; (void)d_ws; (void)ws_size;
-    vae_v14<<<NBLK, NTHR, 0, stream>>>(
+    vae_v16<<<NBLK, NTHR, 0, stream>>>(
         (const float*)d_in[0], (const int*)d_in[1], (const int*)d_in[2], (const float*)d_in[3],
         (const float*)d_in[4], (const float*)d_in[5], (const float*)d_in[6], (const float*)d_in[7],
         (const float*)d_in[8], (const float*)d_in[9], (const float*)d_in[10], (const float*)d_in[11],
```

New measurement: 21.38 ms. 1.74x slower.
